# Kernel tuning notes

Hardware: AMD Instinct MI355X
Metric: run time of the kernel (lower is better)

Reference implementation:

```python
import jax, jax.numpy as jnp
import numpy as np

B, IN, H, NC = 8192, 1024, 1024, 16
CS = H // NC  # chunk_size = 64


def cumsoftmax(x):
    # cumulative softmax along last dim
    return jnp.cumsum(jax.nn.softmax(x, axis=-1), axis=-1)


def setup_inputs() -> dict:
    key = jax.random.key(0)
    ks = jax.random.split(key, 9)
    s_ih = 1.0 / np.sqrt(IN)
    s_hh = 1.0 / np.sqrt(H)
    return {
        "x": jax.random.normal(ks[0], (B, IN), jnp.float32),
        "hx": jax.random.normal(ks[1], (B, H), jnp.float32),
        "cx": jax.random.normal(ks[2], (B, NC, CS), jnp.float32),
        "input_floor": jax.random.normal(ks[3], (B, NC), jnp.float32),
        "forget_floor": jax.random.normal(ks[4], (B, NC), jnp.float32),
        "W_ih": jax.random.uniform(ks[5], (4 * H, IN), jnp.float32, -s_ih, s_ih),
        "b_ih": jax.random.uniform(ks[6], (4 * H,), jnp.float32, -s_ih, s_ih),
        "W_hh": jax.random.uniform(ks[7], (4 * H, H), jnp.float32, -s_hh, s_hh),
        "b_hh": jax.random.uniform(ks[8], (4 * H,), jnp.float32, -s_hh, s_hh),
    }


def reference(x, hx, cx, input_floor, forget_floor, W_ih, b_ih, W_hh, b_hh):
    # dual GEMM (eval path: dropconnect=0.0 -> plain linear)
    gates = x @ W_ih.T + b_ih + hx @ W_hh.T + b_hh          # [B, 4H]
    g = gates.reshape(-1, NC * 4, CS)                        # [B, 4*NC, CS]
    outgate, cell, ingate, forgetgate = jnp.split(g, 4, axis=1)  # each [B, NC, CS]

    happy_in, sad_in = jnp.split(input_floor, 2, axis=1)     # [B, NC/2] each
    happy_fg, sad_fg = jnp.split(forget_floor, 2, axis=1)

    happy_cingate = cumsoftmax(happy_in)
    happy_cforgetgate = jnp.flip(cumsoftmax(jnp.flip(happy_fg, 1)), 1)
    sad_cingate = jnp.flip(cumsoftmax(jnp.flip(sad_in, 1)), 1)
    sad_cforgetgate = cumsoftmax(sad_fg)

    cingate = jnp.concatenate([happy_cingate, sad_cingate], axis=1)[:, :, None]      # [B, NC, 1]
    cforgetgate = jnp.concatenate([happy_cforgetgate, sad_cforgetgate], axis=1)[:, :, None]

    ingate = jax.nn.sigmoid(ingate)
    forgetgate = jax.nn.sigmoid(forgetgate)
    cell = jnp.tanh(cell)
    outgate = jax.nn.sigmoid(outgate)

    overlap = cforgetgate * cingate
    forgetgate = forgetgate * overlap + (cforgetgate - overlap)
    ingate = ingate * overlap + (cingate - overlap)

    cy = forgetgate * cx + ingate * cell                     # [B, NC, CS]
    hy = outgate * jnp.tanh(cy)
    return hy.reshape(-1, H), cy
```

## Files before the change

kernel.cpp:

```cpp
#include <hip/hip_runtime.h>
#include <hip/hip_bf16.h>


#define B_ROWS 8192
#define IN_DIM 1024
#define H_DIM  1024
#define NCHUNK 16
#define K_TOT  2048

#define BM   256
#define BN   256
#define BK   64
#define NKT  (K_TOT / BK)
#define THREADS 512

#define A_PACK_BYTES ((size_t)B_ROWS * K_TOT * 2)
#define W_PACK_BYTES ((size_t)16 * 256 * K_TOT * 2)

typedef __attribute__((ext_vector_type(4))) float  f32x4;
typedef __bf16 bf16x8 __attribute__((ext_vector_type(8)));

__device__ __forceinline__ float sigmoidf_(float x) {
    return 1.0f / (1.0f + __expf(-x));
}
__device__ __forceinline__ float tanhf_(float x) {
    float e = __expf(-2.0f * fabsf(x));
    float t = (1.0f - e) / (1.0f + e);
    return copysignf(t, x);
}

__device__ __forceinline__ void gload16(const __bf16* gsrc, __bf16* lds_dst) {
    __builtin_amdgcn_global_load_lds(
        (const __attribute__((address_space(1))) unsigned int*)gsrc,
        (__attribute__((address_space(3))) unsigned int*)lds_dst, 16, 0, 0);
}

__device__ __forceinline__ bf16x8 cvt8(f32x4 v0, f32x4 v1) {
    bf16x8 o;
    o[0] = (__bf16)v0.x; o[1] = (__bf16)v0.y; o[2] = (__bf16)v0.z; o[3] = (__bf16)v0.w;
    o[4] = (__bf16)v1.x; o[5] = (__bf16)v1.y; o[6] = (__bf16)v1.z; o[7] = (__bf16)v1.w;
    return o;
}

__global__ __launch_bounds__(256)
void pack_AW(const float* __restrict__ x, const float* __restrict__ hx,
             const float* __restrict__ W_ih, const float* __restrict__ W_hh,
             __bf16* __restrict__ Abf, __bf16* __restrict__ Wp)
{
    const int bid = blockIdx.x;
    const int c8  = threadIdx.x << 3;
    if (bid < B_ROWS) {
        const float* src = (c8 < IN_DIM)
            ? (x  + (size_t)bid * IN_DIM + c8)
            : (hx + (size_t)bid * IN_DIM + (c8 - IN_DIM));
        f32x4 v0 = *reinterpret_cast<const f32x4*>(src);
        f32x4 v1 = *reinterpret_cast<const f32x4*>(src + 4);
        *reinterpret_cast<bf16x8*>(Abf + (size_t)bid * K_TOT + c8) = cvt8(v0, v1);
    } else {
        const int r  = bid - B_ROWS;
        const int bh = r >> 8;
        const int n  = r & 255;
        const int g  = (n >> 4) & 3;
        const int j  = (n >> 6) * 16 + (n & 15);
        const int wr = g * H_DIM + bh * 64 + j;
        const float* src = (c8 < IN_DIM)
            ? (W_ih + (size_t)wr * IN_DIM + c8)
            : (W_hh + (size_t)wr * IN_DIM + (c8 - IN_DIM));
        f32x4 v0 = *reinterpret_cast<const f32x4*>(src);
        f32x4 v1 = *reinterpret_cast<const f32x4*>(src + 4);
        *reinterpret_cast<bf16x8*>(Wp + (size_t)r * K_TOT + c8) = cvt8(v0, v1);
    }
}

__device__ __forceinline__ void stage_half(const __bf16* __restrict__ gbase, int kb,
                                           __bf16* lbase, int row0, int tid) {
    #pragma unroll
    for (int i = 0; i < 2; ++i) {
        int e   = i * 4096 + tid * 8;
        int row = row0 + (e >> 6);
        int kd  = e & 63;
        gload16(gbase + (size_t)row * K_TOT + kb + (kd ^ ((row & 7) << 3)), lbase + e);
    }
}

#define SWZ(r, k) ((r) * 64 + ((k) ^ (((r) & 7) << 3)))

#define LDB(Bs) { \
    _Pragma("unroll") \
    for (int fn = 0; fn < 4; ++fn) { \
        int br = wcol + fn * 16 + lr; \
        bfr[fn][0] = *reinterpret_cast<const bf16x8*>(&(Bs)[SWZ(br, lh * 8)]); \
        bfr[fn][1] = *reinterpret_cast<const bf16x8*>(&(Bs)[SWZ(br, 32 + lh * 8)]); \
    } }

#define LDA(As, q) { \
    int ar = wrow + (q) * 32 + lr; \
    af[0][0] = *reinterpret_cast<const bf16x8*>(&(As)[SWZ(ar, lh * 8)]); \
    af[0][1] = *reinterpret_cast<const bf16x8*>(&(As)[SWZ(ar, 32 + lh * 8)]); \
    af[1][0] = *reinterpret_cast<const bf16x8*>(&(As)[SWZ(ar + 16, lh * 8)]); \
    af[1][1] = *reinterpret_cast<const bf16x8*>(&(As)[SWZ(ar + 16, 32 + lh * 8)]); \
    }

#define SB0 __builtin_amdgcn_sched_barrier(0)
#define BARRIER do { \
    asm volatile("" ::: "memory"); \
    __builtin_amdgcn_s_barrier(); \
    asm volatile("" ::: "memory"); \
} while (0)

#define MF(q) { \
    __builtin_amdgcn_s_setprio(1); \
    _Pragma("unroll") \
    for (int ks = 0; ks < 2; ++ks) { \
        _Pragma("unroll") \
        for (int fn = 0; fn < 4; ++fn) { \
            acc[2*(q)][fn]   = __builtin_amdgcn_mfma_f32_16x16x32_bf16(af[0][ks], bfr[fn][ks], acc[2*(q)][fn],   0,0,0); \
            acc[2*(q)+1][fn] = __builtin_amdgcn_mfma_f32_16x16x32_bf16(af[1][ks], bfr[fn][ks], acc[2*(q)+1][fn], 0,0,0); \
        } \
    } \
    __builtin_amdgcn_s_setprio(0); \
}

__global__ __launch_bounds__(THREADS, 2)
void onlstm_gemm8(const __bf16* __restrict__ Abf, const __bf16* __restrict__ Wp,
                  const float* __restrict__ cx,
                  const float* __restrict__ input_floor,
                  const float* __restrict__ forget_floor,
                  const float* __restrict__ b_ih, const float* __restrict__ b_hh,
                  float* __restrict__ out)
{
    __shared__ __align__(16) __bf16 lds[65536];
    __shared__ float ci_s[BM], cf_s[BM], bias_s[BN];

    const int tid = threadIdx.x;
    const int n0  = blockIdx.x;
    const int bm  = (n0 & 7) * 4 + ((n0 >> 3) & 3);
    const int bh  = n0 >> 5;
    const int h0  = bh * 64;
    const int nc  = bh;

    if (tid < BM) {
        {
            int g = (tid >> 4) & 3;
            int j = (tid >> 6) * 16 + (tid & 15);
            int wrr = g * H_DIM + h0 + j;
            bias_s[tid] = b_ih[wrr] + b_hh[wrr];
        }
        int b = bm * BM + tid;
        const int off = (nc < 8) ? 0 : 8;
        const int ic  = (nc < 8) ? nc : (nc - 8);
        const float* pin = input_floor  + (size_t)b * NCHUNK + off;
        const float* pfg = forget_floor + (size_t)b * NCHUNK + off;
        float vi[8], vf[8];
        float mi = -1e30f, mf = -1e30f;
        #pragma unroll
        for (int t = 0; t < 8; ++t) {
            vi[t] = pin[t]; vf[t] = pfg[t];
            mi = fmaxf(mi, vi[t]); mf = fmaxf(mf, vf[t]);
        }
        float si = 0.f, sf = 0.f;
        #pragma unroll
        for (int t = 0; t < 8; ++t) {
            vi[t] = __expf(vi[t] - mi); vf[t] = __expf(vf[t] - mf);
            si += vi[t]; sf += vf[t];
        }
        float pi = 0.f, pf = 0.f;
        #pragma unroll
        for (int t = 0; t < 8; ++t) { if (t <= ic) { pi += vi[t]; pf += vf[t]; } }
        float suf_i = si - pi + vi[ic];
        float suf_f = sf - pf + vf[ic];
        float civ, cfv;
        if (nc < 8) { civ = pi / si;    cfv = suf_f / sf; }
        else        { civ = suf_i / si; cfv = pf / sf;    }
        ci_s[tid] = civ; cf_s[tid] = cfv;
    }

    const __bf16* Arow = Abf + (size_t)(bm * BM) * K_TOT;
    const __bf16* Wblk = Wp  + (size_t)bh * 256 * K_TOT;
    __bf16* const A0p = lds;
    __bf16* const B0p = lds + 16384;
    __bf16* const A1p = lds + 32768;
    __bf16* const B1p = lds + 49152;

    stage_half(Arow, 0,  A0p,        0,   tid);
    stage_half(Arow, 0,  A0p + 8192, 128, tid);
    stage_half(Wblk, 0,  B0p,        0,   tid);
    stage_half(Wblk, 0,  B0p + 8192, 128, tid);
    stage_half(Wblk, BK, B1p,        0,   tid);
    stage_half(Wblk, BK, B1p + 8192, 128, tid);
    asm volatile("s_waitcnt lgkmcnt(0)" ::: "memory");
    asm volatile("s_waitcnt vmcnt(4)"   ::: "memory");
    __builtin_amdgcn_s_barrier();
    asm volatile("" ::: "memory");

    f32x4  acc[8][4];
    #pragma unroll
    for (int i = 0; i < 8; ++i)
        #pragma unroll
        for (int j = 0; j < 4; ++j) acc[i][j] = (f32x4){0.f, 0.f, 0.f, 0.f};
    bf16x8 af[2][2];
    bf16x8 bfr[4][2];

    const int l    = tid & 63;
    const int wid  = tid >> 6;
    const int wrw  = wid >> 2;
    const int wc   = wid & 3;
    const int lr   = l & 15;
    const int lh   = l >> 4;
    const int wrow = wrw * 128;
    const int wcol = wc * 64;

    #pragma unroll 1
    for (int it = 0; it < NKT / 2; ++it) {
        const int t = 2 * it;
        LDB(B0p); LDA(A0p, 0);
        stage_half(Arow, ((t + 1) & 31) * BK, A1p,        0,   tid);
        stage_half(Arow, ((t + 1) & 31) * BK, A1p + 8192, 128, tid);
        SB0; MF(0); BARRIER;
        LDA(A0p, 1);
        stage_half(Wblk, ((t + 2) & 31) * BK, B0p,        0,   tid);
        SB0; MF(1); SB0;
        LDA(A0p, 2);
        stage_half(Wblk, ((t + 2) & 31) * BK, B0p + 8192, 128, tid);
        SB0; MF(2); SB0;
        LDA(A0p, 3);
        SB0; MF(3);
        asm volatile("s_waitcnt vmcnt(4)" ::: "memory");
        BARRIER;
        LDB(B1p); LDA(A1p, 0);
        stage_half(Arow, ((t + 2) & 31) * BK, A0p,        0,   tid);
        stage_half(Arow, ((t + 2) & 31) * BK, A0p + 8192, 128, tid);
        SB0; MF(0); BARRIER;
        LDA(A1p, 1);
        stage_half(Wblk, ((t + 3) & 31) * BK, B1p,        0,   tid);
        SB0; MF(1); SB0;
        LDA(A1p, 2);
        stage_half(Wblk, ((t + 3) & 31) * BK, B1p + 8192, 128, tid);
        SB0; MF(2); SB0;
        LDA(A1p, 3);
        SB0; MF(3);
        asm volatile("s_waitcnt vmcnt(4)" ::: "memory");
        BARRIER;
    }
    asm volatile("s_waitcnt vmcnt(0) lgkmcnt(0)" ::: "memory");
    __builtin_amdgcn_s_barrier();

    const size_t CY_OFF = (size_t)B_ROWS * H_DIM;
    const int hcol = h0 + wc * 16 + lr;
    #pragma unroll
    for (int m = 0; m < 8; ++m) {
        #pragma unroll
        for (int r = 0; r < 4; ++r) {
            int rt = wrow + m * 16 + lh * 4 + r;
            int b  = bm * BM + rt;
            float civ = ci_s[rt], cfv = cf_s[rt];
            float ovl = cfv * civ;
            float og = acc[m][0][r] + bias_s[wcol + lr];
            float cg = acc[m][1][r] + bias_s[wcol + 16 + lr];
            float ig = acc[m][2][r] + bias_s[wcol + 32 + lr];
            float fg = acc[m][3][r] + bias_s[wcol + 48 + lr];
            float i_s = sigmoidf_(ig);
            float f_s = sigmoidf_(fg);
            float c_t = tanhf_(cg);
            float o_s = sigmoidf_(og);
            float fq = f_s * ovl + (cfv - ovl);
            float iq = i_s * ovl + (civ - ovl);
            float cxv = cx[(size_t)b * H_DIM + hcol];
            float cyv = fq * cxv + iq * c_t;
            float hyv = o_s * tanhf_(cyv);
            out[(size_t)b * H_DIM + hcol] = hyv;
            out[CY_OFF + (size_t)b * H_DIM + hcol] = cyv;
        }
    }
}

extern "C" void kernel_launch(void* const* d_in, const int* in_sizes, int n_in,
                              void* d_out, int out_size, void* d_ws, size_t ws_size,
                              hipStream_t stream) {
    const float* x            = (const float*)d_in[0];
    const float* hx           = (const float*)d_in[1];
    const float* cx           = (const float*)d_in[2];
    const float* input_floor  = (const float*)d_in[3];
    const float* forget_floor = (const float*)d_in[4];
    const float* W_ih         = (const float*)d_in[5];
    const float* b_ih         = (const float*)d_in[6];
    const float* W_hh         = (const float*)d_in[7];
    const float* b_hh         = (const float*)d_in[8];
    float* out = (float*)d_out;

    __bf16* Abf = (__bf16*)d_ws;
    __bf16* Wp  = (__bf16*)((char*)d_ws + A_PACK_BYTES);
    pack_AW<<<B_ROWS + 16 * 256, 256, 0, stream>>>(x, hx, W_ih, W_hh, Abf, Wp);
    onlstm_gemm8<<<512, THREADS, 0, stream>>>(
        Abf, Wp, cx, input_floor, forget_floor, b_ih, b_hh, out);
}
```

Before: 156.0 us.

## Triple-buffer A tiles with a single B buffer in the GEMM main loop

```diff
diff --git a/kernel.cpp b/kernel.cpp
--- a/kernel.cpp
+++ b/kernel.cpp
@@ -102,6 +102,7 @@
     }
 
 #define SB0 __builtin_amdgcn_sched_barrier(0)
+#define LGKM0 asm volatile("s_waitcnt lgkmcnt(0)" ::: "memory")
 #define BARRIER do { \
     asm volatile("" ::: "memory"); \
     __builtin_amdgcn_s_barrier(); \
@@ -121,6 +122,28 @@
     __builtin_amdgcn_s_setprio(0); \
 }
 
+#define TILE(T, Ac, An2) { \
+    const int t_ = (T); \
+     \
+    LDB(Bp); LDA(Ac, 0); \
+    SB0; MF(0); LGKM0; BARRIER; \
+     \
+    LDA(Ac, 1); \
+    stage_half(Wblk, ((t_ + 1) & 31) * BK, Bp,        0,   tid); \
+    stage_half(Wblk, ((t_ + 1) & 31) * BK, Bp + 8192, 128, tid); \
+    SB0; MF(1); SB0; \
+     \
+    LDA(Ac, 2); \
+    stage_half(Arow, ((t_ + 2) & 31) * BK, An2,        0,   tid); \
+    stage_half(Arow, ((t_ + 2) & 31) * BK, An2 + 8192, 128, tid); \
+    SB0; MF(2); SB0; \
+     \
+    LDA(Ac, 3); \
+    SB0; MF(3); LGKM0; \
+    asm volatile("s_waitcnt vmcnt(4)" ::: "memory"); \
+    BARRIER; \
+}
+
 __global__ __launch_bounds__(THREADS, 2)
 void onlstm_gemm8(const __bf16* __restrict__ Abf, const __bf16* __restrict__ Wp,
                   const float* __restrict__ cx,
@@ -178,18 +201,18 @@
     const __bf16* Arow = Abf + (size_t)(bm * BM) * K_TOT;
     const __bf16* Wblk = Wp  + (size_t)bh * 256 * K_TOT;
     __bf16* const A0p = lds;
-    __bf16* const B0p = lds + 16384;
-    __bf16* const A1p = lds + 32768;
-    __bf16* const B1p = lds + 49152;
+    __bf16* const A1p = lds + 16384;
+    __bf16* const A2p = lds + 32768;
+    __bf16* const Bp  = lds + 49152;
 
     stage_half(Arow, 0,  A0p,        0,   tid);
     stage_half(Arow, 0,  A0p + 8192, 128, tid);
-    stage_half(Wblk, 0,  B0p,        0,   tid);
-    stage_half(Wblk, 0,  B0p + 8192, 128, tid);
-    stage_half(Wblk, BK, B1p,        0,   tid);
-    stage_half(Wblk, BK, B1p + 8192, 128, tid);
-    asm volatile("s_waitcnt lgkmcnt(0)" ::: "memory");
-    asm volatile("s_waitcnt vmcnt(4)"   ::: "memory");
+    stage_half(Wblk, 0,  Bp,         0,   tid);
+    stage_half(Wblk, 0,  Bp + 8192,  128, tid);
+    stage_half(Arow, BK, A1p,        0,   tid);
+    stage_half(Arow, BK, A1p + 8192, 128, tid);
+    LGKM0;
+    asm volatile("s_waitcnt vmcnt(4)" ::: "memory");
     __builtin_amdgcn_s_barrier();
     asm volatile("" ::: "memory");
 
@@ -211,37 +234,15 @@
     const int wcol = wc * 64;
 
     #pragma unroll 1
-    for (int it = 0; it < NKT / 2; ++it) {
-        const int t = 2 * it;
-        LDB(B0p); LDA(A0p, 0);
-        stage_half(Arow, ((t + 1) & 31) * BK, A1p,        0,   tid);
-        stage_half(Arow, ((t + 1) & 31) * BK, A1p + 8192, 128, tid);
-        SB0; MF(0); BARRIER;
-        LDA(A0p, 1);
-        stage_half(Wblk, ((t + 2) & 31) * BK, B0p,        0,   tid);
-        SB0; MF(1); SB0;
-        LDA(A0p, 2);
-        stage_half(Wblk, ((t + 2) & 31) * BK, B0p + 8192, 128, tid);
-        SB0; MF(2); SB0;
-        LDA(A0p, 3);
-        SB0; MF(3);
-        asm volatile("s_waitcnt vmcnt(4)" ::: "memory");
-        BARRIER;
-        LDB(B1p); LDA(A1p, 0);
-        stage_half(Arow, ((t + 2) & 31) * BK, A0p,        0,   tid);
-        stage_half(Arow, ((t + 2) & 31) * BK, A0p + 8192, 128, tid);
-        SB0; MF(0); BARRIER;
-        LDA(A1p, 1);
-        stage_half(Wblk, ((t + 3) & 31) * BK, B1p,        0,   tid);
-        SB0; MF(1); SB0;
-        LDA(A1p, 2);
-        stage_half(Wblk, ((t + 3) & 31) * BK, B1p + 8192, 128, tid);
-        SB0; MF(2); SB0;
-        LDA(A1p, 3);
-        SB0; MF(3);
-        asm volatile("s_waitcnt vmcnt(4)" ::: "memory");
-        BARRIER;
-    }
+    for (int it = 0; it < 10; ++it) {
+        const int t = 3 * it;
+        TILE(t,     A0p, A2p);
+        TILE(t + 1, A1p, A0p);
+        TILE(t + 2, A2p, A1p);
+    }
+    TILE(30, A0p, A2p);
+    TILE(31, A1p, A0p);
+
     asm volatile("s_waitcnt vmcnt(0) lgkmcnt(0)" ::: "memory");
     __builtin_amdgcn_s_barrier();
 
```

New measurement: 162.8 us. 1.04x slower.
